# Kernel optimization log

Measured on AMD Instinct MI355X. Metric: run time of the kernel, lower is better.

Reference implementation:

```python
import jax, jax.numpy as jnp
import numpy as np
from jax import lax

B, CIN, C, H, W = 16, 512, 64, 64, 160


def flat_softmax(x):
    # softmax over the flattened spatial dims, per (B, C)
    b, c, h, w = x.shape
    return jax.nn.softmax(x.reshape(b, c, h * w), axis=-1).reshape(b, c, h, w)


def dsnt(heatmaps):
    # dsntnn normalized coordinate grid: (2*i + 1)/size - 1, range (-1, 1)
    b, c, h, w = heatmaps.shape
    xs = (2.0 * jnp.arange(w, dtype=heatmaps.dtype) + 1.0) / w - 1.0  # [W]
    ys = (2.0 * jnp.arange(h, dtype=heatmaps.dtype) + 1.0) / h - 1.0  # [H]
    ex = jnp.einsum('bchw,w->bc', heatmaps, xs)
    ey = jnp.einsum('bchw,h->bc', heatmaps, ys)
    return jnp.stack([ex, ey], axis=-1)  # [B, C, 2] as (x, y)


def setup_inputs() -> dict:
    key = jax.random.key(0)
    k1, k2, k3, k4 = jax.random.split(key, 4)
    fcn_out = jax.random.normal(k1, (B, CIN, H, W), dtype=jnp.float32)
    # hm_conv: Conv2d(512, C, 1, bias=False) -> weight [C, 512]
    hm_w = jax.random.normal(k2, (C, CIN), dtype=jnp.float32) * (1.0 / np.sqrt(CIN))
    # heatmap_feature: depthwise 5x5, groups=C -> weight [C, 1, 5, 5]
    dw_w = jax.random.normal(k3, (C, 1, 5, 5), dtype=jnp.float32) * 0.2
    # fushion_conv: 1x1, groups=C -> weight [C, 1, 1, 1] (per-channel scale)
    fu_w = jax.random.normal(k4, (C, 1, 1, 1), dtype=jnp.float32)
    return {"fcn_out": fcn_out, "hm_w": hm_w, "dw_w": dw_w, "fu_w": fu_w}


def _forward(fcn_out, hm_w, dw_w, fu_w):
    # 1x1 conv == channel GEMM
    unnorm = jnp.einsum('bihw,oi->bohw', fcn_out, hm_w)
    heatmaps = flat_softmax(unnorm)
    interme_coords = dsnt(heatmaps)

    # depthwise 5x5 conv, SAME padding
    heatmaps = lax.conv_general_dilated(
        heatmaps, dw_w, window_strides=(1, 1), padding='SAME',
        dimension_numbers=('NCHW', 'OIHW', 'NCHW'), feature_group_count=C)

    b, c, h, w = heatmaps.shape
    feat_a = heatmaps.reshape(b, c, h * w)                    # [B, C, HW]
    relation = jnp.einsum('bcn,bdn->bcd', feat_a, feat_a)     # [B, C, C]
    relation_new = jnp.max(relation, axis=-1, keepdims=True) - relation
    relation = jax.nn.softmax(relation_new, axis=-1)
    feat_e = jnp.einsum('bcd,bdn->bcn', relation, feat_a).reshape(b, c, h, w)
    feature_fushion = feat_e + heatmaps

    # grouped 1x1 conv with groups=C == per-channel scalar scale
    heatmaps = feature_fushion * fu_w[:, 0, :, :][None]       # [C,1,1] broadcast
    heatmaps = flat_softmax(heatmaps)
    final_coords = dsnt(heatmaps)
    return final_coords, interme_coords, heatmaps


def reference(fcn_out, hm_w, dw_w, fu_w):
    return _forward(fcn_out, hm_w, dw_w, fu_w)
```

## Files before the change

kernel.cpp:

```cpp
#include <hip/hip_runtime.h>

#define B_  16
#define CIN 512
#define C_  64
#define H_  64
#define W_  160
#define HW  (H_*W_)
#define NCH 16

typedef __attribute__((ext_vector_type(8))) short bf16x8;
typedef __attribute__((ext_vector_type(4))) float f32x4;
typedef __attribute__((ext_vector_type(8))) unsigned short u16x8;
typedef __attribute__((ext_vector_type(4))) unsigned short u16x4;

__device__ inline unsigned short f2bf(float x) {
    unsigned u = __float_as_uint(x);
    return (unsigned short)((u + 0x7FFF + ((u >> 16) & 1)) >> 16);
}
__device__ inline float bf2f(unsigned short v) {
    return __uint_as_float((unsigned)v << 16);
}

__device__ inline void bf16_split(float x, unsigned short& h, unsigned short& l) {
    h = f2bf(x);
    float lo = x - bf2f(h);
    l = f2bf(lo);
}

__device__ inline void bf16_tsplit(float x, short& h, short& l) {
    unsigned u = __float_as_uint(x);
    h = (short)(u >> 16);
    float hf = __uint_as_float(u & 0xFFFF0000u);
    float lo = x - hf;
    l = (short)(__float_as_uint(lo) >> 16);
}

__global__ __launch_bounds__(256) void k_prep_w(const float* __restrict__ hmw,
                                                unsigned short* __restrict__ wfrag) {
    int tid  = blockIdx.x * 256 + threadIdx.x;
    int j    = tid & 7;
    int lane = (tid >> 3) & 63;
    int t    = (tid >> 9) & 3;
    int p    = (tid >> 11) & 1;
    int ks   = tid >> 12;
    int o = t * 16 + (lane & 15);
    int k = ks * 32 + ((lane >> 4) << 3) + j;
    float val = hmw[o * CIN + k];
    unsigned short h, l;
    bf16_split(val, h, l);
    wfrag[tid] = p ? l : h;
}

__global__ __launch_bounds__(512, 4) void k_gemm1_mfma(const float* __restrict__ fcn,
                                                       const unsigned short* __restrict__ wfrag,
                                                       float* __restrict__ out) {
    const int lane  = threadIdx.x & 63;
    const int wv    = threadIdx.x >> 6;
    const int b     = blockIdx.y;
    const int pxblk = blockIdx.x * 256;

    __shared__ float xs[2][32 * 256];

    const int chl  = (lane >> 4) << 3;
    const int pxw  = wv * 32;
    const int px16 = lane & 15;
    const unsigned short* __restrict__ wp = wfrag + lane * 8;

    const size_t gbase = (size_t)b * CIN * HW + pxblk + (lane << 2);
    const int    grow0 = wv << 2;
    const int    lbase = grow0 * 256;

#define STAGE(buf, ks)                                                                  \
    {                                                                                   \
        _Pragma("unroll")                                                               \
        for (int i = 0; i < 4; ++i) {                                                   \
            const float* g = fcn + gbase + (size_t)((ks) * 32 + grow0 + i) * HW;        \
            float* l = &xs[(buf)][lbase + i * 256];                                     \
            __builtin_amdgcn_global_load_lds(                                           \
                (const __attribute__((address_space(1))) void*)g,                       \
                (__attribute__((address_space(3))) void*)l, 16, 0, 0);                  \
        }                                                                               \
    }

    f32x4 acc[2][4];
#pragma unroll
    for (int xt = 0; xt < 2; ++xt)
#pragma unroll
        for (int t = 0; t < 4; ++t) acc[xt][t] = (f32x4)0.f;

    STAGE(0, 0);
    __syncthreads();

    int cur = 0;
#pragma unroll 1
    for (int ks = 0; ks < 16; ++ks) {
        if (ks < 15) STAGE(cur ^ 1, ks + 1);

        float xa[8], xb[8];
#pragma unroll
        for (int j = 0; j < 8; ++j) {
            const float* r = &xs[cur][(chl + j) * 256 + pxw + px16];
            xa[j] = r[0];
            xb[j] = r[16];
        }
        bf16x8 xah, xal, xbh, xbl;
#pragma unroll
        for (int j = 0; j < 8; ++j) {
            short h, l;
            bf16_tsplit(xa[j], h, l);
            xah[j] = h; xal[j] = l;
            bf16_tsplit(xb[j], h, l);
            xbh[j] = h; xbl[j] = l;
        }
        const unsigned short* __restrict__ wk = wp + (size_t)ks * 4096;
        bf16x8 wh = *reinterpret_cast<const bf16x8*>(wk);
        bf16x8 wl = *reinterpret_cast<const bf16x8*>(wk + 4 * 512);
#pragma unroll
        for (int t = 0; t < 4; ++t) {
            bf16x8 whn, wln;
            if (t < 3) {
                whn = *reinterpret_cast<const bf16x8*>(wk + (t + 1) * 512);
                wln = *reinterpret_cast<const bf16x8*>(wk + (4 + t + 1) * 512);
            }
            acc[0][t] = __builtin_amdgcn_mfma_f32_16x16x32_bf16(wh, xah, acc[0][t], 0, 0, 0);
            acc[0][t] = __builtin_amdgcn_mfma_f32_16x16x32_bf16(wh, xal, acc[0][t], 0, 0, 0);
            acc[0][t] = __builtin_amdgcn_mfma_f32_16x16x32_bf16(wl, xah, acc[0][t], 0, 0, 0);
            acc[1][t] = __builtin_amdgcn_mfma_f32_16x16x32_bf16(wh, xbh, acc[1][t], 0, 0, 0);
            acc[1][t] = __builtin_amdgcn_mfma_f32_16x16x32_bf16(wh, xbl, acc[1][t], 0, 0, 0);
            acc[1][t] = __builtin_amdgcn_mfma_f32_16x16x32_bf16(wl, xbh, acc[1][t], 0, 0, 0);
            wh = whn; wl = wln;
        }

        __syncthreads();
        cur ^= 1;
    }
#undef STAGE

    const int orow = (lane >> 4) << 2;
    float* __restrict__ op = out + (size_t)b * C_ * HW + pxblk + pxw + px16;
#pragma unroll
    for (int xt = 0; xt < 2; ++xt)
#pragma unroll
        for (int t = 0; t < 4; ++t)
#pragma unroll
            for (int reg = 0; reg < 4; ++reg)
                op[(size_t)(t * 16 + orow + reg) * HW + xt * 16] = acc[xt][t][reg];
}

__global__ __launch_bounds__(256) void k_softmax_dsnt_conv(const float* __restrict__ in0,
                                                           const float* __restrict__ dw,
                                                           unsigned short* __restrict__ aout,
                                                           float* __restrict__ coords) {
    const int row = blockIdx.x;
    const int c   = row & (C_ - 1);
    const int tid = threadIdx.x;
    const float4* in04 = reinterpret_cast<const float4*>(in0 + (size_t)row * HW);
    __shared__ float rowbuf[HW];
    __shared__ float red[16];
    float4* r4 = reinterpret_cast<float4*>(rowbuf);

    float m = -3.402823466e38f;
    for (int j = tid; j < HW/4; j += 256) {
        float4 u = in04[j];
        r4[j] = u;
        m = fmaxf(m, fmaxf(fmaxf(u.x, u.y), fmaxf(u.z, u.w)));
    }
#pragma unroll
    for (int off = 32; off > 0; off >>= 1) m = fmaxf(m, __shfl_xor(m, off));
    if ((tid & 63) == 0) red[tid >> 6] = m;
    __syncthreads();
    m = fmaxf(fmaxf(red[0], red[1]), fmaxf(red[2], red[3]));

    const float invw = 1.f / W_, invh = 1.f / H_;
    float s = 0.f, sx = 0.f, sy = 0.f;
    for (int j = tid; j < HW/4; j += 256) {
        float4 u = r4[j];
        int e0 = j * 4;
        int h  = e0 / W_;
        int w0 = e0 - h * W_;
        float y  = (2*h + 1) * invh - 1.f;
        float x0 = (2*w0 + 1) * invw - 1.f;
        float4 e;
        e.x = __expf(u.x - m); s += e.x; sy = fmaf(e.x, y, sy); sx = fmaf(e.x, x0,          sx);
        e.y = __expf(u.y - m); s += e.y; sy = fmaf(e.y, y, sy); sx = fmaf(e.y, x0 + 2*invw, sx);
        e.z = __expf(u.z - m); s += e.z; sy = fmaf(e.z, y, sy); sx = fmaf(e.z, x0 + 4*invw, sx);
        e.w = __expf(u.w - m); s += e.w; sy = fmaf(e.w, y, sy); sx = fmaf(e.w, x0 + 6*invw, sx);
        r4[j] = e;
    }
#pragma unroll
    for (int off = 32; off > 0; off >>= 1) {
        s  += __shfl_xor(s,  off);
        sx += __shfl_xor(sx, off);
        sy += __shfl_xor(sy, off);
    }
    if ((tid & 63) == 0) { int w = tid >> 6; red[4+w] = s; red[8+w] = sx; red[12+w] = sy; }
    __syncthreads();
    s  = red[4] + red[5] + red[6]  + red[7];
    sx = red[8] + red[9] + red[10] + red[11];
    sy = red[12] + red[13] + red[14] + red[15];
    float inv = 1.f / s;

    if (tid == 0) {
        coords[row*2 + 0] = sx * inv;
        coords[row*2 + 1] = sy * inv;
    }

    float wv[25];
#pragma unroll
    for (int k = 0; k < 25; ++k) wv[k] = dw[c * 25 + k];

    u16x4* aout4 = reinterpret_cast<u16x4*>(aout + (size_t)row * HW);
    for (int j = tid; j < HW/4; j += 256) {
        int h  = j / (W_/4);
        int w4 = j - h * (W_/4);
        int w4m = (w4 > 0) ? w4 - 1 : 0;
        int w4p = (w4 < W_/4 - 1) ? w4 + 1 : W_/4 - 1;
        float a0 = 0.f, a1 = 0.f, a2 = 0.f, a3 = 0.f;
#pragma unroll
        for (int dy = 0; dy < 5; ++dy) {
            int rr = h + dy - 2;
            bool rok = (rr >= 0) && (rr < H_);
            int rc = rok ? rr : 0;
            const float4* rp = reinterpret_cast<const float4*>(rowbuf + rc * W_);
            float4 L = rp[w4m];
            float4 M = rp[w4];
            float4 R = rp[w4p];
            float f[12];
            f[0]=L.x; f[1]=L.y; f[2]=L.z; f[3]=L.w;
            f[4]=M.x; f[5]=M.y; f[6]=M.z; f[7]=M.w;
            f[8]=R.x; f[9]=R.y; f[10]=R.z; f[11]=R.w;
            if (!rok) {
#pragma unroll
                for (int q = 0; q < 12; ++q) f[q] = 0.f;
            }
            if (w4 == 0)          { f[0]=f[1]=f[2]=f[3] = 0.f; }
            if (w4 == W_/4 - 1)   { f[8]=f[9]=f[10]=f[11] = 0.f; }
            const float* wr = wv + dy * 5;
#pragma unroll
            for (int dx = 0; dx < 5; ++dx) {
                float wt = wr[dx];
                a0 = fmaf(f[2 + 0 + dx], wt, a0);
                a1 = fmaf(f[2 + 1 + dx], wt, a1);
                a2 = fmaf(f[2 + 2 + dx], wt, a2);
                a3 = fmaf(f[2 + 3 + dx], wt, a3);
            }
        }
        u16x4 ov;
        ov[0] = f2bf(a0 * inv); ov[1] = f2bf(a1 * inv);
        ov[2] = f2bf(a2 * inv); ov[3] = f2bf(a3 * inv);
        aout4[j] = ov;
    }
}

__global__ __launch_bounds__(256) void k_rel_partial(const unsigned short* __restrict__ A,
                                                     float* __restrict__ part) {
    const int b  = blockIdx.y, ch = blockIdx.x;
    const int lane = threadIdx.x & 63;
    const int w    = threadIdx.x >> 6;
    const int hwb  = ch * (HW / NCH);
    const unsigned short* __restrict__ ab = A + (size_t)b * C_ * HW;
    const int r16 = lane & 15, h8 = (lane >> 4) << 3;
    const unsigned short* __restrict__ own = ab + (size_t)(w * 16 + r16) * HW;

    f32x4 acc[4];
#pragma unroll
    for (int d = 0; d < 4; ++d) acc[d] = (f32x4)0.f;

#pragma unroll 1
    for (int kk = 0; kk < (HW / NCH) / 32; ++kk) {
        const int hw0 = hwb + kk * 32 + h8;
        bf16x8 fra = *reinterpret_cast<const bf16x8*>(own + hw0);
#pragma unroll
        for (int d = 0; d < 4; ++d) {
            bf16x8 frb = *reinterpret_cast<const bf16x8*>(ab + (size_t)(d * 16 + r16) * HW + hw0);
            acc[d] = __builtin_amdgcn_mfma_f32_16x16x32_bf16(fra, frb, acc[d], 0, 0, 0);
        }
    }

    float* __restrict__ pp = part + (size_t)(b * NCH + ch) * 4096;
    const int crow = w * 16 + ((lane >> 4) << 2);
#pragma unroll
    for (int d = 0; d < 4; ++d)
#pragma unroll
        for (int reg = 0; reg < 4; ++reg)
            pp[(crow + reg) * 64 + d * 16 + r16] = acc[d][reg];
}

__global__ __launch_bounds__(256) void k_rel_finalize(const float* __restrict__ part,
                                                      unsigned short* __restrict__ rfrag) {
    const int b = blockIdx.x;
    __shared__ float rel[64][65];
    __shared__ float Rs[64][64];
    for (int e = threadIdx.x; e < 4096; e += 256) {
        float s = 0.f;
        for (int k = 0; k < NCH; ++k) s += part[(size_t)(b * NCH + k) * 4096 + e];
        rel[e >> 6][e & 63] = s;
    }
    __syncthreads();
    if (threadIdx.x < 64) {
        int cc = threadIdx.x;
        float mn = rel[cc][0];
        for (int d = 1; d < 64; ++d) mn = fminf(mn, rel[cc][d]);
        float s = 0.f;
        for (int d = 0; d < 64; ++d) s += __expf(mn - rel[cc][d]);
        float inv = 1.f / s;
        for (int d = 0; d < 64; ++d)
            Rs[cc][d] = __expf(mn - rel[cc][d]) * inv;
    }
    __syncthreads();
    unsigned short* __restrict__ rb = rfrag + (size_t)b * 8192;
    for (int idx = threadIdx.x; idx < 1024; idx += 256) {
        int lane = idx & 63;
        int rest = idx >> 6;
        int t  = rest & 3;
        int p  = (rest >> 2) & 1;
        int ks = rest >> 3;
        int o  = t * 16 + (lane & 15);
        int d0 = ks * 32 + ((lane >> 4) << 3);
        bf16x8 v;
#pragma unroll
        for (int j = 0; j < 8; ++j) {
            unsigned short h, l;
            bf16_split(Rs[o][d0 + j], h, l);
            v[j] = (short)(p ? l : h);
        }
        *reinterpret_cast<bf16x8*>(rb + idx * 8) = v;
    }
}

__global__ __launch_bounds__(256, 4) void k_feate_mfma(const unsigned short* __restrict__ A,
                                                       const unsigned short* __restrict__ rfrag,
                                                       const float* __restrict__ fu,
                                                       unsigned short* __restrict__ tout) {
    const int lane = threadIdx.x & 63;
    const int wv   = threadIdx.x >> 6;
    const int b    = blockIdx.y;
    const int px0  = blockIdx.x * 128 + wv * 32;

    const int pxa = px0 + (lane & 15);
    const int chl = (lane >> 4) << 3;
    const unsigned short* __restrict__ apx = A + ((size_t)b * C_ + chl) * HW + pxa;
    const unsigned short* __restrict__ rp = rfrag + (size_t)b * 8192 + lane * 8;

    f32x4 acc[2][4];
#pragma unroll
    for (int xt = 0; xt < 2; ++xt)
#pragma unroll
        for (int t = 0; t < 4; ++t) acc[xt][t] = (f32x4)0.f;

#pragma unroll 1
    for (int ks = 0; ks < 2; ++ks) {
        bf16x8 xa, xb;
#pragma unroll
        for (int j = 0; j < 8; ++j) {
            const unsigned short* p0 = apx + (size_t)(ks * 32 + j) * HW;
            xa[j] = (short)p0[0];
            xb[j] = (short)p0[16];
        }
        const unsigned short* __restrict__ rk = rp + (size_t)ks * 8 * 512;
        bf16x8 rh = *reinterpret_cast<const bf16x8*>(rk);
        bf16x8 rl = *reinterpret_cast<const bf16x8*>(rk + 4 * 512);
#pragma unroll
        for (int t = 0; t < 4; ++t) {
            bf16x8 rhn, rln;
            if (t < 3) {
                rhn = *reinterpret_cast<const bf16x8*>(rk + (t + 1) * 512);
                rln = *reinterpret_cast<const bf16x8*>(rk + (4 + t + 1) * 512);
            }
            acc[0][t] = __builtin_amdgcn_mfma_f32_16x16x32_bf16(rh, xa, acc[0][t], 0, 0, 0);
            acc[0][t] = __builtin_amdgcn_mfma_f32_16x16x32_bf16(rl, xa, acc[0][t], 0, 0, 0);
            acc[1][t] = __builtin_amdgcn_mfma_f32_16x16x32_bf16(rh, xb, acc[1][t], 0, 0, 0);
            acc[1][t] = __builtin_amdgcn_mfma_f32_16x16x32_bf16(rl, xb, acc[1][t], 0, 0, 0);
            rh = rhn; rl = rln;
        }
    }

    const int orow = (lane >> 4) << 2;
    const unsigned short* __restrict__ ares = A + (size_t)b * C_ * HW + px0 + (lane & 15);
    unsigned short* __restrict__ op        = tout + (size_t)b * C_ * HW + px0 + (lane & 15);
#pragma unroll
    for (int xt = 0; xt < 2; ++xt)
#pragma unroll
        for (int t = 0; t < 4; ++t)
#pragma unroll
            for (int reg = 0; reg < 4; ++reg) {
                const int oc = t * 16 + orow + reg;
                float r = acc[xt][t][reg] + bf2f(ares[(size_t)oc * HW + xt * 16]);
                op[(size_t)oc * HW + xt * 16] = f2bf(r * fu[oc]);
            }
}

__global__ __launch_bounds__(256) void k_softmax_dsnt(const unsigned short* __restrict__ in0,
                                                      float* __restrict__ pout,
                                                      float* __restrict__ coords) {
    const int row = blockIdx.x;
    const int tid = threadIdx.x;
    const u16x8* in08 = reinterpret_cast<const u16x8*>(in0 + (size_t)row * HW);
    float4*      out4 = reinterpret_cast<float4*>(pout + (size_t)row * HW);
    __shared__ float rowbuf[HW];
    __shared__ float red[16];
    float4* r4 = reinterpret_cast<float4*>(rowbuf);

    float m = -3.402823466e38f;
    for (int j = tid; j < HW/8; j += 256) {
        u16x8 u = in08[j];
        float4 a, bv;
        a.x  = bf2f(u[0]); a.y  = bf2f(u[1]); a.z  = bf2f(u[2]); a.w  = bf2f(u[3]);
        bv.x = bf2f(u[4]); bv.y = bf2f(u[5]); bv.z = bf2f(u[6]); bv.w = bf2f(u[7]);
        r4[2*j]     = a;
        r4[2*j + 1] = bv;
        m = fmaxf(m, fmaxf(fmaxf(a.x, a.y), fmaxf(a.z, a.w)));
        m = fmaxf(m, fmaxf(fmaxf(bv.x, bv.y), fmaxf(bv.z, bv.w)));
    }
#pragma unroll
    for (int off = 32; off > 0; off >>= 1) m = fmaxf(m, __shfl_xor(m, off));
    if ((tid & 63) == 0) red[tid >> 6] = m;
    __syncthreads();
    m = fmaxf(fmaxf(red[0], red[1]), fmaxf(red[2], red[3]));

    const float invw = 1.f / W_, invh = 1.f / H_;
    float s = 0.f, sx = 0.f, sy = 0.f;
    for (int j = tid; j < HW/4; j += 256) {
        float4 u = r4[j];
        int e0 = j * 4;
        int h  = e0 / W_;
        int w0 = e0 - h * W_;
        float y  = (2*h + 1) * invh - 1.f;
        float x0 = (2*w0 + 1) * invw - 1.f;
        float4 e;
        e.x = __expf(u.x - m); s += e.x; sy = fmaf(e.x, y, sy); sx = fmaf(e.x, x0,          sx);
        e.y = __expf(u.y - m); s += e.y; sy = fmaf(e.y, y, sy); sx = fmaf(e.y, x0 + 2*invw, sx);
        e.z = __expf(u.z - m); s += e.z; sy = fmaf(e.z, y, sy); sx = fmaf(e.z, x0 + 4*invw, sx);
        e.w = __expf(u.w - m); s += e.w; sy = fmaf(e.w, y, sy); sx = fmaf(e.w, x0 + 6*invw, sx);
        r4[j] = e;
    }
#pragma unroll
    for (int off = 32; off > 0; off >>= 1) {
        s  += __shfl_xor(s,  off);
        sx += __shfl_xor(sx, off);
        sy += __shfl_xor(sy, off);
    }
    if ((tid & 63) == 0) { int w = tid >> 6; red[4+w] = s; red[8+w] = sx; red[12+w] = sy; }
    __syncthreads();
    s  = red[4] + red[5] + red[6]  + red[7];
    sx = red[8] + red[9] + red[10] + red[11];
    sy = red[12] + red[13] + red[14] + red[15];
    float inv = 1.f / s;

    for (int j = tid; j < HW/4; j += 256) {
        float4 e = r4[j];
        e.x *= inv; e.y *= inv; e.z *= inv; e.w *= inv;
        out4[j] = e;
    }
    if (tid == 0) {
        coords[row*2 + 0] = sx * inv;
        coords[row*2 + 1] = sy * inv;
    }
}

extern "C" void kernel_launch(void* const* d_in, const int* in_sizes, int n_in,
                              void* d_out, int out_size, void* d_ws, size_t ws_size,
                              hipStream_t stream) {
    const float* fcn = (const float*)d_in[0];
    const float* hmw = (const float*)d_in[1];
    const float* dww = (const float*)d_in[2];
    const float* fuw = (const float*)d_in[3];
    float* out = (float*)d_out;
    char* ws = (char*)d_ws;

    size_t off = 0;
    unsigned short* wfrag = (unsigned short*)(ws + off); off += 131072;
    float*          buf1  = (float*)         (ws + off); off += 41943040;
    unsigned short* abf   = (unsigned short*)(ws + off); off += 20971520;
    float*          part  = (float*)         (ws + off); off += (size_t)NCH*16*4096*4;
    unsigned short* rfrag = (unsigned short*)(ws + off); off += 262144;
    unsigned short* tbuf  = (unsigned short*)(ws + off); off += 20971520;

    float* hm2            = out + 4096;
    float* final_coords   = out;
    float* interme_coords = out + 2048;

    hipLaunchKernelGGL(k_prep_w,            dim3(256),      dim3(256), 0, stream, hmw, wfrag);
    hipLaunchKernelGGL(k_gemm1_mfma,        dim3(40, 16),   dim3(512), 0, stream, fcn, wfrag, buf1);
    hipLaunchKernelGGL(k_softmax_dsnt_conv, dim3(1024),     dim3(256), 0, stream, buf1, dww, abf, interme_coords);
    hipLaunchKernelGGL(k_rel_partial,       dim3(NCH, 16),  dim3(256), 0, stream, abf, part);
    hipLaunchKernelGGL(k_rel_finalize,      dim3(16),       dim3(256), 0, stream, part, rfrag);
    hipLaunchKernelGGL(k_feate_mfma,        dim3(80, 16),   dim3(256), 0, stream, abf, rfrag, fuw, tbuf);
    hipLaunchKernelGGL(k_softmax_dsnt,      dim3(1024),     dim3(256), 0, stream, tbuf, hm2, final_coords);
}
```

Before: 194.4 us.

## Fuse relation partial GEMM and softmax finalize into one per-batch kernel

Merges the split-K relation Gram kernel and the finalize kernel into a single kernel with one 1024-thread block per batch. Four K-chunks are reduced in LDS instead of through a global partial buffer. The finalize kernel's 16-way partial sum then becomes a 4-way sum read from shared memory. This removes a launch and the global round trip for partials, but cuts the grid from 256 blocks to 16, so the read of the 20 MB activation runs on only 16 CUs.

Result: slower. 350.8 us (+80.4%).

```diff
diff --git a/kernel.cpp b/kernel.cpp
--- a/kernel.cpp
+++ b/kernel.cpp
@@ -6,7 +6,6 @@
 #define H_  64
 #define W_  160
 #define HW  (H_*W_)
-#define NCH 16
 
 typedef __attribute__((ext_vector_type(8))) short bf16x8;
 typedef __attribute__((ext_vector_type(4))) float f32x4;
@@ -252,23 +251,28 @@
     }
 }
 
-__global__ __launch_bounds__(256) void k_rel_partial(const unsigned short* __restrict__ A,
-                                                     float* __restrict__ part) {
-    const int b  = blockIdx.y, ch = blockIdx.x;
-    const int lane = threadIdx.x & 63;
-    const int w    = threadIdx.x >> 6;
-    const int hwb  = ch * (HW / NCH);
+__global__ __launch_bounds__(1024) void k_relation(const unsigned short* __restrict__ A,
+                                                   unsigned short* __restrict__ rfrag) {
+    const int b    = blockIdx.x;
+    const int tid  = threadIdx.x;
+    const int lane = tid & 63;
+    const int w    = tid >> 6;
+    const int cg   = w & 3;
+    const int kc   = w >> 2;
     const unsigned short* __restrict__ ab = A + (size_t)b * C_ * HW;
     const int r16 = lane & 15, h8 = (lane >> 4) << 3;
-    const unsigned short* __restrict__ own = ab + (size_t)(w * 16 + r16) * HW;
+    const unsigned short* __restrict__ own = ab + (size_t)(cg * 16 + r16) * HW;
+
+    __shared__ float rel4[4][64][64];
+    __shared__ float Rs[64][64];
 
     f32x4 acc[4];
 #pragma unroll
     for (int d = 0; d < 4; ++d) acc[d] = (f32x4)0.f;
 
 #pragma unroll 1
-    for (int kk = 0; kk < (HW / NCH) / 32; ++kk) {
-        const int hw0 = hwb + kk * 32 + h8;
+    for (int kk = 0; kk < 80; ++kk) {
+        const int hw0 = kc * 2560 + kk * 32 + h8;
         bf16x8 fra = *reinterpret_cast<const bf16x8*>(own + hw0);
 #pragma unroll
         for (int d = 0; d < 4; ++d) {
@@ -277,40 +281,36 @@
         }
     }
 
-    float* __restrict__ pp = part + (size_t)(b * NCH + ch) * 4096;
-    const int crow = w * 16 + ((lane >> 4) << 2);
+    const int crow = cg * 16 + ((lane >> 4) << 2);
 #pragma unroll
     for (int d = 0; d < 4; ++d)
 #pragma unroll
         for (int reg = 0; reg < 4; ++reg)
-            pp[(crow + reg) * 64 + d * 16 + r16] = acc[d][reg];
-}
-
-__global__ __launch_bounds__(256) void k_rel_finalize(const float* __restrict__ part,
-                                                      unsigned short* __restrict__ rfrag) {
-    const int b = blockIdx.x;
-    __shared__ float rel[64][65];
-    __shared__ float Rs[64][64];
-    for (int e = threadIdx.x; e < 4096; e += 256) {
+            rel4[kc][crow + reg][d * 16 + r16] = acc[d][reg];
+    __syncthreads();
+
+    if (tid < 64) {
+        int cc = tid;
+        float rowv[64];
+        float mn = 3.402823466e38f;
+#pragma unroll 4
+        for (int d = 0; d < 64; ++d) {
+            float s = rel4[0][cc][d] + rel4[1][cc][d] + rel4[2][cc][d] + rel4[3][cc][d];
+            rowv[d] = s;
+            mn = fminf(mn, s);
+        }
         float s = 0.f;
-        for (int k = 0; k < NCH; ++k) s += part[(size_t)(b * NCH + k) * 4096 + e];
-        rel[e >> 6][e & 63] = s;
-    }
-    __syncthreads();
-    if (threadIdx.x < 64) {
-        int cc = threadIdx.x;
-        float mn = rel[cc][0];
-        for (int d = 1; d < 64; ++d) mn = fminf(mn, rel[cc][d]);
-        float s = 0.f;
-        for (int d = 0; d < 64; ++d) s += __expf(mn - rel[cc][d]);
+#pragma unroll 4
+        for (int d = 0; d < 64; ++d) s += __expf(mn - rowv[d]);
         float inv = 1.f / s;
+#pragma unroll 4
         for (int d = 0; d < 64; ++d)
-            Rs[cc][d] = __expf(mn - rel[cc][d]) * inv;
-    }
-    __syncthreads();
-    unsigned short* __restrict__ rb = rfrag + (size_t)b * 8192;
-    for (int idx = threadIdx.x; idx < 1024; idx += 256) {
-        int lane = idx & 63;
+            Rs[cc][d] = __expf(mn - rowv[d]) * inv;
+    }
+    __syncthreads();
+
+    {
+        int idx  = tid;
         int rest = idx >> 6;
         int t  = rest & 3;
         int p  = (rest >> 2) & 1;
@@ -324,7 +324,7 @@
             bf16_split(Rs[o][d0 + j], h, l);
             v[j] = (short)(p ? l : h);
         }
-        *reinterpret_cast<bf16x8*>(rb + idx * 8) = v;
+        *reinterpret_cast<bf16x8*>(rfrag + (size_t)b * 8192 + idx * 8) = v;
     }
 }
 
@@ -472,7 +472,6 @@
     unsigned short* wfrag = (unsigned short*)(ws + off); off += 131072;
     float*          buf1  = (float*)         (ws + off); off += 41943040;
     unsigned short* abf   = (unsigned short*)(ws + off); off += 20971520;
-    float*          part  = (float*)         (ws + off); off += (size_t)NCH*16*4096*4;
     unsigned short* rfrag = (unsigned short*)(ws + off); off += 262144;
     unsigned short* tbuf  = (unsigned short*)(ws + off); off += 20971520;
 
@@ -480,11 +479,10 @@
     float* final_coords   = out;
     float* interme_coords = out + 2048;
 
-    hipLaunchKernelGGL(k_prep_w,            dim3(256),      dim3(256), 0, stream, hmw, wfrag);
-    hipLaunchKernelGGL(k_gemm1_mfma,        dim3(40, 16),   dim3(512), 0, stream, fcn, wfrag, buf1);
-    hipLaunchKernelGGL(k_softmax_dsnt_conv, dim3(1024),     dim3(256), 0, stream, buf1, dww, abf, interme_coords);
-    hipLaunchKernelGGL(k_rel_partial,       dim3(NCH, 16),  dim3(256), 0, stream, abf, part);
-    hipLaunchKernelGGL(k_rel_finalize,      dim3(16),       dim3(256), 0, stream, part, rfrag);
-    hipLaunchKernelGGL(k_feate_mfma,        dim3(80, 16),   dim3(256), 0, stream, abf, rfrag, fuw, tbuf);
-    hipLaunchKernelGGL(k_softmax_dsnt,      dim3(1024),     dim3(256), 0, stream, tbuf, hm2, final_coords);
-}
+    hipLaunchKernelGGL(k_prep_w,            dim3(256),      dim3(256),  0, stream, hmw, wfrag);
+    hipLaunchKernelGGL(k_gemm1_mfma,        dim3(40, 16),   dim3(512),  0, stream, fcn, wfrag, buf1);
+    hipLaunchKernelGGL(k_softmax_dsnt_conv, dim3(1024),     dim3(256),  0, stream, buf1, dww, abf, interme_coords);
+    hipLaunchKernelGGL(k_relation,          dim3(16),       dim3(1024), 0, stream, abf, rfrag);
+    hipLaunchKernelGGL(k_feate_mfma,        dim3(80, 16),   dim3(256),  0, stream, abf, rfrag, fuw, tbuf);
+    hipLaunchKernelGGL(k_softmax_dsnt,      dim3(1024),     dim3(256),  0, stream, tbuf, hm2, final_coords);
+}
```

## Stage GEMM weight fragments through LDS and use explicit vmcnt pipeline waits

Applied to the files above, without the earlier changes.

Weight fragments for each K-step are now copied into a double-buffered LDS array with global_load_lds, alongside the activation tile, instead of being read from global memory by every wave. The loop replaces __syncthreads with explicit s_waitcnt vmcnt(5) plus s_barrier, so the next stage's loads can stay in flight while the current buffer is consumed, and the last iteration is peeled. This is meant to cut redundant global weight traffic and load latency on the MFMA path. It adds LDS usage that may lower occupancy, and it depends on the hand-counted vmcnt being correct.

New measurement: 178.7 us. -8.1%, faster.

```diff
diff --git a/kernel.cpp b/kernel.cpp
--- a/kernel.cpp
+++ b/kernel.cpp
@@ -60,11 +60,11 @@
     const int pxblk = blockIdx.x * 256;
 
     __shared__ float xs[2][32 * 256];
+    __shared__ unsigned short wsh[2][4096];
 
     const int chl  = (lane >> 4) << 3;
     const int pxw  = wv * 32;
     const int px16 = lane & 15;
-    const unsigned short* __restrict__ wp = wfrag + lane * 8;
 
     const size_t gbase = (size_t)b * CIN * HW + pxblk + (lane << 2);
     const int    grow0 = wv << 2;
@@ -80,6 +80,13 @@
                 (const __attribute__((address_space(1))) void*)g,                       \
                 (__attribute__((address_space(3))) void*)l, 16, 0, 0);                  \
         }                                                                               \
+        {                                                                               \
+            const unsigned short* g = wfrag + (ks) * 4096 + wv * 512 + lane * 8;        \
+            unsigned short* l = &wsh[(buf)][wv * 512];                                  \
+            __builtin_amdgcn_global_load_lds(                                           \
+                (const __attribute__((address_space(1))) void*)g,                       \
+                (__attribute__((address_space(3))) void*)l, 16, 0, 0);                  \
+        }                                                                               \
     }
 
     f32x4 acc[2][4];
@@ -88,53 +95,66 @@
 #pragma unroll
         for (int t = 0; t < 4; ++t) acc[xt][t] = (f32x4)0.f;
 
+#define COMPUTE(bb)                                                                     \
+    {                                                                                   \
+        float xa[8], xb[8];                                                             \
+        _Pragma("unroll")                                                               \
+        for (int j = 0; j < 8; ++j) {                                                   \
+            const float* r = &xs[(bb)][(chl + j) * 256 + pxw + px16];                   \
+            xa[j] = r[0];                                                               \
+            xb[j] = r[16];                                                              \
+        }                                                                               \
+        bf16x8 xah, xal, xbh, xbl;                                                      \
+        _Pragma("unroll")                                                               \
+        for (int j = 0; j < 8; ++j) {                                                   \
+            short h, l;                                                                 \
+            bf16_tsplit(xa[j], h, l);                                                   \
+            xah[j] = h; xal[j] = l;                                                     \
+            bf16_tsplit(xb[j], h, l);                                                   \
+            xbh[j] = h; xbl[j] = l;                                                     \
+        }                                                                               \
+        const unsigned short* wk = &wsh[(bb)][0];                                       \
+        bf16x8 wh = *reinterpret_cast<const bf16x8*>(wk + (lane << 3));                 \
+        bf16x8 wl = *reinterpret_cast<const bf16x8*>(wk + ((4 * 64 + lane) << 3));      \
+        _Pragma("unroll")                                                               \
+        for (int t = 0; t < 4; ++t) {                                                   \
+            bf16x8 whn, wln;                                                            \
+            if (t < 3) {                                                                \
+                whn = *reinterpret_cast<const bf16x8*>(wk + (((t + 1) * 64 + lane) << 3)); \
+                wln = *reinterpret_cast<const bf16x8*>(wk + (((5 + t) * 64 + lane) << 3)); \
+            }                                                                           \
+            acc[0][t] = __builtin_amdgcn_mfma_f32_16x16x32_bf16(wh, xah, acc[0][t], 0, 0, 0); \
+            acc[0][t] = __builtin_amdgcn_mfma_f32_16x16x32_bf16(wh, xal, acc[0][t], 0, 0, 0); \
+            acc[0][t] = __builtin_amdgcn_mfma_f32_16x16x32_bf16(wl, xah, acc[0][t], 0, 0, 0); \
+            acc[1][t] = __builtin_amdgcn_mfma_f32_16x16x32_bf16(wh, xbh, acc[1][t], 0, 0, 0); \
+            acc[1][t] = __builtin_amdgcn_mfma_f32_16x16x32_bf16(wh, xbl, acc[1][t], 0, 0, 0); \
+            acc[1][t] = __builtin_amdgcn_mfma_f32_16x16x32_bf16(wl, xbh, acc[1][t], 0, 0, 0); \
+            wh = whn; wl = wln;                                                         \
+        }                                                                               \
+    }
+
     STAGE(0, 0);
-    __syncthreads();
+    asm volatile("s_waitcnt vmcnt(0)" ::: "memory");
+    __builtin_amdgcn_sched_barrier(0);
+    __builtin_amdgcn_s_barrier();
 
     int cur = 0;
 #pragma unroll 1
-    for (int ks = 0; ks < 16; ++ks) {
-        if (ks < 15) STAGE(cur ^ 1, ks + 1);
-
-        float xa[8], xb[8];
-#pragma unroll
-        for (int j = 0; j < 8; ++j) {
-            const float* r = &xs[cur][(chl + j) * 256 + pxw + px16];
-            xa[j] = r[0];
-            xb[j] = r[16];
-        }
-        bf16x8 xah, xal, xbh, xbl;
-#pragma unroll
-        for (int j = 0; j < 8; ++j) {
-            short h, l;
-            bf16_tsplit(xa[j], h, l);
-            xah[j] = h; xal[j] = l;
-            bf16_tsplit(xb[j], h, l);
-            xbh[j] = h; xbl[j] = l;
-        }
-        const unsigned short* __restrict__ wk = wp + (size_t)ks * 4096;
-        bf16x8 wh = *reinterpret_cast<const bf16x8*>(wk);
-        bf16x8 wl = *reinterpret_cast<const bf16x8*>(wk + 4 * 512);
-#pragma unroll
-        for (int t = 0; t < 4; ++t) {
-            bf16x8 whn, wln;
-            if (t < 3) {
-                whn = *reinterpret_cast<const bf16x8*>(wk + (t + 1) * 512);
-                wln = *reinterpret_cast<const bf16x8*>(wk + (4 + t + 1) * 512);
-            }
-            acc[0][t] = __builtin_amdgcn_mfma_f32_16x16x32_bf16(wh, xah, acc[0][t], 0, 0, 0);
-            acc[0][t] = __builtin_amdgcn_mfma_f32_16x16x32_bf16(wh, xal, acc[0][t], 0, 0, 0);
-            acc[0][t] = __builtin_amdgcn_mfma_f32_16x16x32_bf16(wl, xah, acc[0][t], 0, 0, 0);
-            acc[1][t] = __builtin_amdgcn_mfma_f32_16x16x32_bf16(wh, xbh, acc[1][t], 0, 0, 0);
-            acc[1][t] = __builtin_amdgcn_mfma_f32_16x16x32_bf16(wh, xbl, acc[1][t], 0, 0, 0);
-            acc[1][t] = __builtin_amdgcn_mfma_f32_16x16x32_bf16(wl, xbh, acc[1][t], 0, 0, 0);
-            wh = whn; wl = wln;
-        }
-
-        __syncthreads();
+    for (int ks = 0; ks < 15; ++ks) {
+        STAGE(cur ^ 1, ks + 1);
+        asm volatile("s_waitcnt vmcnt(5)" ::: "memory");
+        __builtin_amdgcn_sched_barrier(0);
+        __builtin_amdgcn_s_barrier();
+        COMPUTE(cur);
+        __builtin_amdgcn_s_barrier();
         cur ^= 1;
     }
+    asm volatile("s_waitcnt vmcnt(0)" ::: "memory");
+    __builtin_amdgcn_sched_barrier(0);
+    __builtin_amdgcn_s_barrier();
+    COMPUTE(cur);
 #undef STAGE
+#undef COMPUTE
 
     const int orow = (lane >> 4) << 2;
     float* __restrict__ op = out + (size_t)b * C_ * HW + pxblk + pxw + px16;
```
